# Kernel tuning notes

Measured on AMD Instinct MI355X. Metric: run time of the kernel, lower is better.

## Reference

```python
import jax, jax.numpy as jnp
import numpy as np

EMBED_DIM = 128
N_HEADS = 8
HEAD_DEPTH = EMBED_DIM // N_HEADS  # 16
CLIP = 10.0
B, N = 256, 1000


def setup_inputs() -> dict:
    key = jax.random.key(0)
    ks = jax.random.split(key, 10)
    D = EMBED_DIM
    return {
        "node_embeddings": jax.random.normal(ks[0], (B, N, D), jnp.float32),
        "graph_embedding": jax.random.normal(ks[1], (B, D), jnp.float32),
        "step_context": jax.random.normal(ks[2], (B, 1, D + 2), jnp.float32),
        "mask": jax.random.randint(ks[3], (B, 1, N), 0, 2).astype(bool),
        "Wk1": jax.random.normal(ks[4], (D, D), jnp.float32) / np.sqrt(D),
        "Wv": jax.random.normal(ks[5], (D, D), jnp.float32) / np.sqrt(D),
        "Wk2": jax.random.normal(ks[6], (D, D), jnp.float32) / np.sqrt(D),
        "Wq_fixed": jax.random.normal(ks[7], (D, D), jnp.float32) / np.sqrt(D),
        "Wout": jax.random.normal(ks[8], (D, D), jnp.float32) / np.sqrt(D),
        "Wq_step": jax.random.normal(ks[9], (D + 2, D), jnp.float32) / np.sqrt(D),
    }


def reference(node_embeddings, graph_embedding, step_context, mask,
              Wk1, Wv, Wk2, Wq_fixed, Wout, Wq_step):
    b, n, D = node_embeddings.shape
    H, dh = N_HEADS, HEAD_DEPTH
    neg_inf = jnp.float32(-1e9)

    # compute_static: precomputed projections of node/graph embeddings
    K1 = node_embeddings @ Wk1                      # [B,N,D]
    V = node_embeddings @ Wv                        # [B,N,D]
    K2 = node_embeddings @ Wk2                      # [B,N,D]
    Q_fixed = graph_embedding[:, None, :] @ Wq_fixed  # [B,1,D]

    # compute_dynamic: single-query masked MHA
    Q_step = step_context @ Wq_step                 # [B,1,D]
    Q1 = Q_fixed + Q_step                           # [B,1,D]
    q = Q1.reshape(b, 1, H, dh)
    k = K1.reshape(b, n, H, dh)
    v = V.reshape(b, n, H, dh)
    score = jnp.einsum('bqhd,bkhd->bhqk', q, k) / jnp.sqrt(jnp.float32(dh))
    score = jnp.where(mask[:, None, :, :], neg_inf, score)  # mask [B,1,N] -> [B,1,1,N]
    attn = jax.nn.softmax(score, axis=-1)           # [B,H,1,N]
    mha = jnp.einsum('bhqk,bkhd->bqhd', attn, v).reshape(b, 1, D)
    Q2 = mha @ Wout                                 # [B,1,D]

    # SHA: clipped single-head logits over all nodes
    logits = CLIP * jnp.tanh(
        jnp.einsum('bqd,bkd->bqk', Q2, K2) / jnp.sqrt(jnp.float32(D)))  # [B,1,N]
    logits = jnp.where(mask, neg_inf, logits)
    return logits[:, 0, :]                          # [B,N]
```

## Files before the change

### kernel.cpp

```cpp
#include <hip/hip_runtime.h>
#include <stdint.h>


#define DD 128
#define NH 8
#define DHD 16
#define NS 8
#define TILE 64
#define RP 132
#define SP 9
#define NMAX_PAD 1024

__device__ __forceinline__ bool detect_mask32(const void* maskp) {
    const uint32_t* mw = (const uint32_t*)maskp;
    bool m32 = true;
    #pragma unroll
    for (int i = 0; i < 16; ++i) m32 = m32 && (mw[i] <= 1u);
    return m32;
}

__global__ __launch_bounds__(128)
void k0_prep(const float* __restrict__ graph, const float* __restrict__ ctx,
             const float* __restrict__ Wk1, const float* __restrict__ Wqf,
             const float* __restrict__ Wqs, float* __restrict__ wq_ws)
{
    __shared__ float q1[DD];
    const int b = blockIdx.x, tid = threadIdx.x;
    const float* ge = graph + (size_t)b * DD;
    const float* sc = ctx + (size_t)b * (DD + 2);
    float acc = 0.f;
    #pragma unroll 4
    for (int k = 0; k < DD; ++k)     acc += ge[k] * Wqf[k * DD + tid];
    #pragma unroll 4
    for (int k = 0; k < DD + 2; ++k) acc += sc[k] * Wqs[k * DD + tid];
    q1[tid] = acc;
    __syncthreads();
    const float* wrow = Wk1 + (size_t)tid * DD;
    #pragma unroll
    for (int h = 0; h < NH; ++h) {
        float a = 0.f;
        #pragma unroll
        for (int j = 0; j < DHD; ++j) a += wrow[h * DHD + j] * q1[h * DHD + j];
        wq_ws[(size_t)b * NH * DD + h * DD + tid] = 0.25f * a;
    }
}

__global__ __launch_bounds__(512)
void kA_flash(const float* __restrict__ node, const float* __restrict__ wq_ws,
              const void* __restrict__ maskp, float* __restrict__ spart_ws,
              float* __restrict__ mz_ws, int N)
{
    __shared__ float tile[TILE * RP];
    __shared__ float wq_l[NH * RP];
    __shared__ float s_t[TILE * SP];
    const int b = blockIdx.y, j = blockIdx.x, tid = threadIdx.x;
    const int lane = tid & 63, h = tid >> 6;
    const int rows = (N + NS - 1) / NS;
    const int n0 = j * rows;
    const int nend = min(n0 + rows, N);
    const bool m32 = detect_mask32(maskp);
    const int32_t* mi = (const int32_t*)maskp + (size_t)b * N;
    const uint8_t* mb = (const uint8_t*)maskp + (size_t)b * N;
    const float* nodeB = node + (size_t)b * N * DD;

    for (int i = tid; i < NH * DD; i += 512)
        wq_l[(i >> 7) * RP + (i & 127)] = wq_ws[(size_t)b * NH * DD + i];

    const int r_sc = tid >> 3, h_sc = tid & 7;
    float m_run = -1e9f, z_run = 0.f;
    float accx = 0.f, accy = 0.f;

    const int ntiles = (nend - n0 + TILE - 1) / TILE;
    for (int t = 0; t < ntiles; ++t) {
        const int nt0 = n0 + t * TILE;
        #pragma unroll
        for (int c = 0; c < 4; ++c) {
            const int idx = c * 2048 + tid * 4;
            const int row = idx >> 7, col = idx & 127;
            if (nt0 + row < nend)
                *(float4*)&tile[row * RP + col] =
                    *(const float4*)(nodeB + (size_t)(nt0 + row) * DD + col);
        }
        __syncthreads();
        {
            const int n = nt0 + r_sc;
            float sc = -1e9f;
            if (n < nend) {
                const bool m = m32 ? (mi[n] != 0) : (mb[n] != 0);
                if (!m) {
                    const float4* nr = (const float4*)&tile[r_sc * RP];
                    const float4* wr = (const float4*)&wq_l[h_sc * RP];
                    float a = 0.f;
                    #pragma unroll
                    for (int k = 0; k < 32; ++k) {
                        const float4 x = nr[k], w = wr[k];
                        a += x.x * w.x + x.y * w.y + x.z * w.z + x.w * w.w;
                    }
                    sc = a;
                }
            }
            s_t[r_sc * SP + h_sc] = sc;
        }
        __syncthreads();
        {
            float scl = s_t[lane * SP + h];
            float tmax = scl;
            #pragma unroll
            for (int d = 1; d < 64; d <<= 1) tmax = fmaxf(tmax, __shfl_xor(tmax, d));
            const float m_new = fmaxf(m_run, tmax);
            const float rescale = __expf(m_run - m_new);
            const float e = __expf(scl - m_new);
            s_t[lane * SP + h] = e;
            float zt = e;
            #pragma unroll
            for (int d = 1; d < 64; d <<= 1) zt += __shfl_xor(zt, d);
            z_run = z_run * rescale + zt;
            accx *= rescale;
            accy *= rescale;
            m_run = m_new;
        }
        #pragma unroll 8
        for (int r = 0; r < TILE; ++r) {
            const float ef = s_t[r * SP + h];
            const float2 v = *(const float2*)&tile[r * RP + 2 * lane];
            accx += ef * v.x;
            accy += ef * v.y;
        }
        __syncthreads();
    }
    float* vout = spart_ws + (((size_t)b * NS + j) * NH + h) * DD;
    vout[2 * lane]     = accx;
    vout[2 * lane + 1] = accy;
    if (lane == 0) {
        float* mzp = mz_ws + (((size_t)b * NS + j) * NH + h) * 2;
        mzp[0] = m_run;
        mzp[1] = z_run;
    }
}

__global__ __launch_bounds__(128)
void kB_combine(const float* __restrict__ spart_ws, const float* __restrict__ mz_ws,
                const float* __restrict__ Wv, const float* __restrict__ Wout,
                const float* __restrict__ Wk2, float* __restrict__ w2_ws)
{
    __shared__ float m_l[NH * NS], z_l[NH * NS], wt[NH * NS];
    __shared__ float s_l[NH * DD];
    __shared__ float mha_l[DD];
    __shared__ float q2_l[DD];
    const int b = blockIdx.x, tid = threadIdx.x;

    if (tid < NH * NS) {
        const int h = tid >> 3, j = tid & 7;
        const float* mzp = mz_ws + (((size_t)b * NS + j) * NH + h) * 2;
        m_l[h * NS + j] = mzp[0];
        z_l[h * NS + j] = mzp[1];
    }
    __syncthreads();
    if (tid < NH) {
        const int h = tid;
        float M = -1e30f;
        #pragma unroll
        for (int j = 0; j < NS; ++j) M = fmaxf(M, m_l[h * NS + j]);
        float w[NS], Z = 0.f;
        #pragma unroll
        for (int j = 0; j < NS; ++j) {
            w[j] = __expf(m_l[h * NS + j] - M);
            Z += z_l[h * NS + j] * w[j];
        }
        const float rz = 1.f / Z;
        #pragma unroll
        for (int j = 0; j < NS; ++j) wt[h * NS + j] = w[j] * rz;
    }
    __syncthreads();
    const float* sp = spart_ws + (size_t)b * NS * NH * DD;
    for (int o = tid; o < NH * DD; o += 128) {
        const int h = o >> 7;
        float s = 0.f;
        #pragma unroll
        for (int j = 0; j < NS; ++j)
            s += sp[(size_t)j * NH * DD + o] * wt[h * NS + j];
        s_l[o] = s;
    }
    __syncthreads();
    {
        const int h = tid >> 4;
        float a = 0.f;
        for (int dp = 0; dp < DD; ++dp) a += s_l[h * DD + dp] * Wv[dp * DD + tid];
        mha_l[tid] = a;
    }
    __syncthreads();
    {
        float a = 0.f;
        for (int e = 0; e < DD; ++e) a += mha_l[e] * Wout[e * DD + tid];
        q2_l[tid] = a;
    }
    __syncthreads();
    {
        const float4* row = (const float4*)(Wk2 + (size_t)tid * DD);
        float a = 0.f;
        #pragma unroll
        for (int k = 0; k < 32; ++k) {
            const float4 w = row[k];
            a += w.x * q2_l[4*k] + w.y * q2_l[4*k+1] + w.z * q2_l[4*k+2] + w.w * q2_l[4*k+3];
        }
        w2_ws[(size_t)b * DD + tid] = a * 0.08838834764831845f;
    }
}

__global__ __launch_bounds__(256)
void k5_logits(const float* __restrict__ node, const float* __restrict__ w2_ws,
               const void* __restrict__ maskp, float* __restrict__ out, int N)
{
    const int b = blockIdx.y, j = blockIdx.x, tid = threadIdx.x;
    const int rows = (N + NS - 1) / NS;
    const int n0 = j * rows;
    const int nend = min(n0 + rows, N);
    const bool m32 = detect_mask32(maskp);
    const int32_t* mi = (const int32_t*)maskp + (size_t)b * N;
    const uint8_t* mb = (const uint8_t*)maskp + (size_t)b * N;
    const int sub = tid & 7, rr = tid >> 3;

    const float4* wv = (const float4*)(w2_ws + (size_t)b * DD + sub * 16);
    const float4 w0 = wv[0], w1 = wv[1], w2v = wv[2], w3 = wv[3];
    const float* nodeB = node + (size_t)b * N * DD;
    float* outB = out + (size_t)b * N;

    for (int n = n0 + rr; n < nend; n += 32) {
        const float4* nr = (const float4*)(nodeB + (size_t)n * DD + sub * 16);
        const float4 a0 = nr[0], a1 = nr[1], a2 = nr[2], a3 = nr[3];
        float p = a0.x*w0.x + a0.y*w0.y + a0.z*w0.z + a0.w*w0.w
                + a1.x*w1.x + a1.y*w1.y + a1.z*w1.z + a1.w*w1.w
                + a2.x*w2v.x + a2.y*w2v.y + a2.z*w2v.z + a2.w*w2v.w
                + a3.x*w3.x + a3.y*w3.y + a3.z*w3.z + a3.w*w3.w;
        p += __shfl_xor(p, 1);
        p += __shfl_xor(p, 2);
        p += __shfl_xor(p, 4);
        if (sub == 0) {
            const bool m = m32 ? (mi[n] != 0) : (mb[n] != 0);
            const float t = 1.f - 2.f / (__expf(2.f * p) + 1.f);
            outB[n] = m ? -1e9f : 10.f * t;
        }
    }
}

#define TPB 512
#define NMAX 1000
#define SPAD 9

__global__ __launch_bounds__(TPB)
void decoder_fallback(const float* __restrict__ node, const float* __restrict__ graph,
                      const float* __restrict__ ctx, const void* __restrict__ maskp,
                      const float* __restrict__ Wk1, const float* __restrict__ Wv,
                      const float* __restrict__ Wk2, const float* __restrict__ Wqf,
                      const float* __restrict__ Wout, const float* __restrict__ Wqs,
                      float* __restrict__ out, int N)
{
    __shared__ float node_tile[TILE * RP];
    __shared__ float scores[NMAX * SPAD];
    __shared__ float wq[NH * RP];
    __shared__ float s_lds[NH * RP];
    __shared__ float q1[DD];
    __shared__ float mha[DD];
    __shared__ float q2[DD];
    __shared__ float w2[DD];

    const int b = blockIdx.x, tid = threadIdx.x, lane = tid & 63, wave = tid >> 6;
    const bool mask32 = detect_mask32(maskp);
    const int32_t* mi = (const int32_t*)maskp + (size_t)b * N;
    const uint8_t* mb = (const uint8_t*)maskp + (size_t)b * N;
    const float* nodeB = node + (size_t)b * N * DD;

    if (tid < DD) {
        const float* ge = graph + (size_t)b * DD;
        const float* sc = ctx + (size_t)b * (DD + 2);
        float acc = 0.f;
        for (int k = 0; k < DD; ++k)     acc += ge[k] * Wqf[k * DD + tid];
        for (int k = 0; k < DD + 2; ++k) acc += sc[k] * Wqs[k * DD + tid];
        q1[tid] = acc;
    }
    __syncthreads();
    for (int idx = tid; idx < NH * DD; idx += TPB) {
        const int h = idx >> 7, dp = idx & (DD - 1);
        const float* wrow = Wk1 + dp * DD + h * DHD;
        float acc = 0.f;
        #pragma unroll
        for (int j = 0; j < DHD; ++j) acc += wrow[j] * q1[h * DHD + j];
        wq[h * RP + dp] = 0.25f * acc;
    }
    __syncthreads();
    const int ntiles = (N + TILE - 1) / TILE;
    const int n_local = tid >> 3, hA = tid & 7;
    for (int t = 0; t < ntiles; ++t) {
        const int n0 = t * TILE;
        #pragma unroll
        for (int c = 0; c < 4; ++c) {
            const int idx = c * (TPB * 4) + tid * 4;
            const int row = idx >> 7, col = idx & (DD - 1);
            if (n0 + row < N)
                *(float4*)&node_tile[row * RP + col] =
                    *(const float4*)(nodeB + (size_t)(n0 + row) * DD + col);
        }
        __syncthreads();
        if (n0 + n_local < N) {
            const float4* nr = (const float4*)&node_tile[n_local * RP];
            const float4* wr = (const float4*)&wq[hA * RP];
            float acc = 0.f;
            #pragma unroll
            for (int k = 0; k < DD / 4; ++k) {
                const float4 a = nr[k], w = wr[k];
                acc += a.x * w.x + a.y * w.y + a.z * w.z + a.w * w.w;
            }
            scores[(n0 + n_local) * SPAD + hA] = acc;
        }
        __syncthreads();
    }
    {
        const int h = wave;
        float sm[16];
        #pragma unroll
        for (int k = 0; k < 16; ++k) {
            const int n = lane + 64 * k;
            float v = -1e9f;
            if (n < N) {
                const bool m = mask32 ? (mi[n] != 0) : (mb[n] != 0);
                v = m ? -1e9f : scores[n * SPAD + h];
            }
            sm[k] = v;
        }
        float mx = sm[0];
        #pragma unroll
        for (int k = 1; k < 16; ++k) mx = fmaxf(mx, sm[k]);
        #pragma unroll
        for (int d = 1; d < 64; d <<= 1) mx = fmaxf(mx, __shfl_xor(mx, d));
        float e[16];
        float sum = 0.f;
        #pragma unroll
        for (int k = 0; k < 16; ++k) {
            const int n = lane + 64 * k;
            e[k] = (n < N) ? __expf(sm[k] - mx) : 0.f;
            sum += e[k];
        }
        #pragma unroll
        for (int d = 1; d < 64; d <<= 1) sum += __shfl_xor(sum, d);
        const float rinv = 1.f / sum;
        #pragma unroll
        for (int k = 0; k < 16; ++k) {
            const int n = lane + 64 * k;
            if (n < N) scores[n * SPAD + h] = e[k] * rinv;
        }
    }
    __syncthreads();
    {
        const int h = wave;
        const float2* n2 = (const float2*)nodeB;
        float a0 = 0.f, a1 = 0.f;
        #pragma unroll 4
        for (int n = 0; n < N; ++n) {
            const float at = scores[n * SPAD + h];
            const float2 v = n2[(size_t)n * 64 + lane];
            a0 += at * v.x;
            a1 += at * v.y;
        }
        s_lds[h * RP + 2 * lane] = a0;
        s_lds[h * RP + 2 * lane + 1] = a1;
    }
    __syncthreads();
    if (tid < DD) {
        const int h = tid >> 4;
        float acc = 0.f;
        for (int dp = 0; dp < DD; ++dp) acc += s_lds[h * RP + dp] * Wv[dp * DD + tid];
        mha[tid] = acc;
    }
    __syncthreads();
    if (tid < DD) {
        float acc = 0.f;
        for (int e = 0; e < DD; ++e) acc += mha[e] * Wout[e * DD + tid];
        q2[tid] = acc;
    }
    __syncthreads();
    if (tid < DD) {
        const float4* row = (const float4*)(Wk2 + tid * DD);
        float acc = 0.f;
        #pragma unroll
        for (int k = 0; k < DD / 4; ++k) {
            const float4 wv = row[k];
            acc += wv.x * q2[4*k] + wv.y * q2[4*k+1] + wv.z * q2[4*k+2] + wv.w * q2[4*k+3];
        }
        w2[tid] = acc * 0.08838834764831845f;
    }
    __syncthreads();
    {
        const float wa = w2[2 * lane], wb = w2[2 * lane + 1];
        const float2* n2 = (const float2*)nodeB;
        float* outB = out + (size_t)b * N;
        for (int n = wave; n < N; n += NH) {
            const float2 v = n2[(size_t)n * 64 + lane];
            float p = v.x * wa + v.y * wb;
            #pragma unroll
            for (int d = 1; d < 64; d <<= 1) p += __shfl_xor(p, d);
            if (lane == 0) {
                const bool m = mask32 ? (mi[n] != 0) : (mb[n] != 0);
                const float t = 1.f - 2.f / (__expf(2.f * p) + 1.f);
                outB[n] = m ? -1e9f : 10.f * t;
            }
        }
    }
}

extern "C" void kernel_launch(void* const* d_in, const int* in_sizes, int n_in,
                              void* d_out, int out_size, void* d_ws, size_t ws_size,
                              hipStream_t stream) {
    (void)n_in; (void)out_size;
    const float* node  = (const float*)d_in[0];
    const float* graph = (const float*)d_in[1];
    const float* ctx   = (const float*)d_in[2];
    const void*  mask  = d_in[3];
    const float* Wk1   = (const float*)d_in[4];
    const float* Wv    = (const float*)d_in[5];
    const float* Wk2   = (const float*)d_in[6];
    const float* Wqf   = (const float*)d_in[7];
    const float* Wout  = (const float*)d_in[8];
    const float* Wqs   = (const float*)d_in[9];

    const int B = in_sizes[1] / DD;
    const int N = in_sizes[0] / (B * DD);

    const size_t off_wq    = 0;
    const size_t off_spart = off_wq + (size_t)B * NH * DD;
    const size_t off_mz    = off_spart + (size_t)B * NS * NH * DD;
    const size_t off_w2    = off_mz + (size_t)B * NS * NH * 2;
    const size_t need_f    = off_w2 + (size_t)B * DD;

    if (N <= NMAX_PAD && ws_size >= need_f * sizeof(float)) {
        float* ws       = (float*)d_ws;
        float* wq_ws    = ws + off_wq;
        float* spart_ws = ws + off_spart;
        float* mz_ws    = ws + off_mz;
        float* w2_ws    = ws + off_w2;

        k0_prep<<<B, 128, 0, stream>>>(graph, ctx, Wk1, Wqf, Wqs, wq_ws);
        kA_flash<<<dim3(NS, B), 512, 0, stream>>>(node, wq_ws, mask, spart_ws, mz_ws, N);
        kB_combine<<<B, 128, 0, stream>>>(spart_ws, mz_ws, Wv, Wout, Wk2, w2_ws);
        k5_logits<<<dim3(NS, B), 256, 0, stream>>>(node, w2_ws, mask, (float*)d_out, N);
    } else {
        decoder_fallback<<<B, TPB, 0, stream>>>(node, graph, ctx, mask,
                                                Wk1, Wv, Wk2, Wqf, Wout, Wqs,
                                                (float*)d_out, N);
    }
}
```

Baseline: 118.6 us.

## Rewrite attention split kernel with bf16 MFMA for scores and PV

Replaces the scalar FP32 flash-style attention partial kernel with one that converts the node tile to bf16 in shared memory and uses 16x16x32 bf16 MFMA instructions for both the Q·K scores and the softmax-weighted V sum. Each block now loads its whole 125-row chunk at once and does a single-pass softmax with block-wide max and sum reductions, instead of an online rescaling loop over 64-row tiles. The goal is to move the FP32 ALU dot products onto matrix cores. In exchange, scores and probabilities are rounded to bf16, the code assumes at most 128 rows per split, and the transposed B-fragment gather for PV reads shared memory with strided scalar loads.

```diff
diff --git a/kernel.cpp b/kernel.cpp
--- a/kernel.cpp
+++ b/kernel.cpp
@@ -10,6 +10,15 @@
 #define RP 132
 #define SP 9
 #define NMAX_PAD 1024
+
+typedef short v8s __attribute__((ext_vector_type(8)));
+typedef float v4f __attribute__((ext_vector_type(4)));
+
+__device__ __forceinline__ unsigned short f2bf(float x) {
+    unsigned u = __float_as_uint(x);
+    u += 0x7fffu + ((u >> 16) & 1u);
+    return (unsigned short)(u >> 16);
+}
 
 __device__ __forceinline__ bool detect_mask32(const void* maskp) {
     const uint32_t* mw = (const uint32_t*)maskp;
@@ -46,95 +55,164 @@
 }
 
 __global__ __launch_bounds__(512)
-void kA_flash(const float* __restrict__ node, const float* __restrict__ wq_ws,
-              const void* __restrict__ maskp, float* __restrict__ spart_ws,
-              float* __restrict__ mz_ws, int N)
+void kA_mfma(const float* __restrict__ node, const float* __restrict__ wq_ws,
+             const void* __restrict__ maskp, float* __restrict__ spart_ws,
+             float* __restrict__ mz_ws, int N)
 {
-    __shared__ float tile[TILE * RP];
-    __shared__ float wq_l[NH * RP];
-    __shared__ float s_t[TILE * SP];
+    __shared__ __align__(16) unsigned short tA[2][8][64][16];
+    __shared__ __align__(16) unsigned short Ph[2][16][72];
+    __shared__ float wmax[16][9];
+    __shared__ float zpart[16][9];
+    __shared__ float mfin[16];
+
     const int b = blockIdx.y, j = blockIdx.x, tid = threadIdx.x;
-    const int lane = tid & 63, h = tid >> 6;
+    const int lane = tid & 63, w = tid >> 6;
+    const int c = lane & 15, g = lane >> 4;
     const int rows = (N + NS - 1) / NS;
     const int n0 = j * rows;
     const int nend = min(n0 + rows, N);
+
+    if (nend <= n0) {
+        float* sp = spart_ws + ((size_t)b * NS + j) * NH * DD;
+        for (int o = tid; o < NH * DD; o += 512) sp[o] = 0.f;
+        if (tid < NH) {
+            float* mzp = mz_ws + (((size_t)b * NS + j) * NH + tid) * 2;
+            mzp[0] = -1e30f; mzp[1] = 0.f;
+        }
+        return;
+    }
+
     const bool m32 = detect_mask32(maskp);
     const int32_t* mi = (const int32_t*)maskp + (size_t)b * N;
     const uint8_t* mb = (const uint8_t*)maskp + (size_t)b * N;
     const float* nodeB = node + (size_t)b * N * DD;
 
-    for (int i = tid; i < NH * DD; i += 512)
-        wq_l[(i >> 7) * RP + (i & 127)] = wq_ws[(size_t)b * NH * DD + i];
-
-    const int r_sc = tid >> 3, h_sc = tid & 7;
-    float m_run = -1e9f, z_run = 0.f;
-    float accx = 0.f, accy = 0.f;
-
-    const int ntiles = (nend - n0 + TILE - 1) / TILE;
-    for (int t = 0; t < ntiles; ++t) {
-        const int nt0 = n0 + t * TILE;
-        #pragma unroll
-        for (int c = 0; c < 4; ++c) {
-            const int idx = c * 2048 + tid * 4;
-            const int row = idx >> 7, col = idx & 127;
-            if (nt0 + row < nend)
-                *(float4*)&tile[row * RP + col] =
-                    *(const float4*)(nodeB + (size_t)(nt0 + row) * DD + col);
-        }
-        __syncthreads();
-        {
-            const int n = nt0 + r_sc;
-            float sc = -1e9f;
+    v8s aw[4];
+    #pragma unroll
+    for (int kk = 0; kk < 4; ++kk) {
+        v8s a;
+        #pragma unroll
+        for (int i = 0; i < 8; ++i) a[i] = 0;
+        if (c < NH) {
+            const float* wr = wq_ws + (size_t)b * NH * DD + (size_t)c * DD + kk * 32 + g * 8;
+            #pragma unroll
+            for (int i = 0; i < 8; ++i) a[i] = (short)f2bf(wr[i]);
+        }
+        aw[kk] = a;
+    }
+
+    {
+        const int L = tid >> 3, c8 = tid & 7;
+        #pragma unroll
+        for (int t = 0; t < 2; ++t) {
+            const int n = n0 + t * 64 + L;
+            unsigned short tmp[16];
             if (n < nend) {
-                const bool m = m32 ? (mi[n] != 0) : (mb[n] != 0);
-                if (!m) {
-                    const float4* nr = (const float4*)&tile[r_sc * RP];
-                    const float4* wr = (const float4*)&wq_l[h_sc * RP];
-                    float a = 0.f;
-                    #pragma unroll
-                    for (int k = 0; k < 32; ++k) {
-                        const float4 x = nr[k], w = wr[k];
-                        a += x.x * w.x + x.y * w.y + x.z * w.z + x.w * w.w;
-                    }
-                    sc = a;
+                const float4* src = (const float4*)(nodeB + (size_t)n * DD + c8 * 16);
+                #pragma unroll
+                for (int k = 0; k < 4; ++k) {
+                    const float4 v = src[k];
+                    tmp[4*k+0] = f2bf(v.x); tmp[4*k+1] = f2bf(v.y);
+                    tmp[4*k+2] = f2bf(v.z); tmp[4*k+3] = f2bf(v.w);
                 }
+            } else {
+                #pragma unroll
+                for (int k = 0; k < 16; ++k) tmp[k] = 0;
             }
-            s_t[r_sc * SP + h_sc] = sc;
-        }
-        __syncthreads();
-        {
-            float scl = s_t[lane * SP + h];
-            float tmax = scl;
-            #pragma unroll
-            for (int d = 1; d < 64; d <<= 1) tmax = fmaxf(tmax, __shfl_xor(tmax, d));
-            const float m_new = fmaxf(m_run, tmax);
-            const float rescale = __expf(m_run - m_new);
-            const float e = __expf(scl - m_new);
-            s_t[lane * SP + h] = e;
-            float zt = e;
-            #pragma unroll
-            for (int d = 1; d < 64; d <<= 1) zt += __shfl_xor(zt, d);
-            z_run = z_run * rescale + zt;
-            accx *= rescale;
-            accy *= rescale;
-            m_run = m_new;
-        }
-        #pragma unroll 8
-        for (int r = 0; r < TILE; ++r) {
-            const float ef = s_t[r * SP + h];
-            const float2 v = *(const float2*)&tile[r * RP + 2 * lane];
-            accx += ef * v.x;
-            accy += ef * v.y;
-        }
-        __syncthreads();
-    }
-    float* vout = spart_ws + (((size_t)b * NS + j) * NH + h) * DD;
-    vout[2 * lane]     = accx;
-    vout[2 * lane + 1] = accy;
-    if (lane == 0) {
-        float* mzp = mz_ws + (((size_t)b * NS + j) * NH + h) * 2;
-        mzp[0] = m_run;
-        mzp[1] = z_run;
+            *(v8s*)&tA[t][c8][L][0] = *(v8s*)&tmp[0];
+            *(v8s*)&tA[t][c8][L][8] = *(v8s*)&tmp[8];
+        }
+    }
+    __syncthreads();
+
+    const int ts = w >> 2, rg = w & 3;
+    const int nrow = n0 + ts * 64 + rg * 16 + c;
+    v4f sc = {0.f, 0.f, 0.f, 0.f};
+    #pragma unroll
+    for (int kk = 0; kk < 4; ++kk) {
+        const v8s bfrag = *(const v8s*)&tA[ts][kk * 2 + (g >> 1)][rg * 16 + c][(g & 1) * 8];
+        sc = __builtin_amdgcn_mfma_f32_16x16x32_bf16(aw[kk], bfrag, sc, 0, 0, 0);
+    }
+
+    float s4[4];
+    {
+        const bool valid = nrow < nend;
+        const bool msk = valid && (m32 ? (mi[nrow] != 0) : (mb[nrow] != 0));
+        #pragma unroll
+        for (int r = 0; r < 4; ++r)
+            s4[r] = !valid ? -1e30f : (msk ? -1e9f : sc[r]);
+    }
+
+    {
+        float mx[4];
+        #pragma unroll
+        for (int r = 0; r < 4; ++r) mx[r] = s4[r];
+        #pragma unroll
+        for (int d = 1; d < 16; d <<= 1) {
+            #pragma unroll
+            for (int r = 0; r < 4; ++r) mx[r] = fmaxf(mx[r], __shfl_xor(mx[r], d));
+        }
+        if (c == 0) {
+            #pragma unroll
+            for (int r = 0; r < 4; ++r) wmax[g * 4 + r][w] = mx[r];
+        }
+    }
+    __syncthreads();
+    if (w == 0 && lane < 16) {
+        float m = wmax[lane][0];
+        #pragma unroll
+        for (int ww = 1; ww < 8; ++ww) m = fmaxf(m, wmax[lane][ww]);
+        mfin[lane] = m;
+    }
+    __syncthreads();
+
+    {
+        float e4[4];
+        #pragma unroll
+        for (int r = 0; r < 4; ++r) e4[r] = __expf(s4[r] - mfin[g * 4 + r]);
+        float zr[4];
+        #pragma unroll
+        for (int r = 0; r < 4; ++r) zr[r] = e4[r];
+        #pragma unroll
+        for (int d = 1; d < 16; d <<= 1) {
+            #pragma unroll
+            for (int r = 0; r < 4; ++r) zr[r] += __shfl_xor(zr[r], d);
+        }
+        if (c == 0) {
+            #pragma unroll
+            for (int r = 0; r < 4; ++r) zpart[g * 4 + r][w] = zr[r];
+        }
+        #pragma unroll
+        for (int r = 0; r < 4; ++r)
+            Ph[ts][g * 4 + r][rg * 16 + c] = f2bf(e4[r]);
+    }
+    __syncthreads();
+
+    v4f c2 = {0.f, 0.f, 0.f, 0.f};
+    #pragma unroll
+    for (int s = 0; s < 4; ++s) {
+        const int t2 = s >> 1, s1 = s & 1;
+        const v8s pa = *(const v8s*)&Ph[t2][c][s1 * 32 + g * 8];
+        v8s bb;
+        #pragma unroll
+        for (int i = 0; i < 8; ++i)
+            bb[i] = (short)tA[t2][w][s1 * 32 + g * 8 + i][c];
+        c2 = __builtin_amdgcn_mfma_f32_16x16x32_bf16(pa, bb, c2, 0, 0, 0);
+    }
+
+    if (g < 2) {
+        float* sp = spart_ws + ((size_t)b * NS + j) * NH * DD;
+        #pragma unroll
+        for (int r = 0; r < 4; ++r)
+            sp[(g * 4 + r) * DD + w * 16 + c] = c2[r];
+    }
+    if (w == 0 && lane < NH) {
+        float z = 0.f;
+        #pragma unroll
+        for (int ww = 0; ww < 8; ++ww) z += zpart[lane][ww];
+        float* mzp = mz_ws + (((size_t)b * NS + j) * NH + lane) * 2;
+        mzp[0] = mfin[lane];
+        mzp[1] = z;
     }
 }
 
@@ -293,8 +371,8 @@
     for (int t = 0; t < ntiles; ++t) {
         const int n0 = t * TILE;
         #pragma unroll
-        for (int c = 0; c < 4; ++c) {
-            const int idx = c * (TPB * 4) + tid * 4;
+        for (int cc = 0; cc < 4; ++cc) {
+            const int idx = cc * (TPB * 4) + tid * 4;
             const int row = idx >> 7, col = idx & (DD - 1);
             if (n0 + row < N)
                 *(float4*)&node_tile[row * RP + col] =
@@ -307,8 +385,8 @@
             float acc = 0.f;
             #pragma unroll
             for (int k = 0; k < DD / 4; ++k) {
-                const float4 a = nr[k], w = wr[k];
-                acc += a.x * w.x + a.y * w.y + a.z * w.z + a.w * w.w;
+                const float4 a = nr[k], wv = wr[k];
+                acc += a.x * wv.x + a.y * wv.y + a.z * wv.z + a.w * wv.w;
             }
             scores[(n0 + n_local) * SPAD + hA] = acc;
         }
@@ -439,7 +517,7 @@
         float* w2_ws    = ws + off_w2;
 
         k0_prep<<<B, 128, 0, stream>>>(graph, ctx, Wk1, Wqf, Wqs, wq_ws);
-        kA_flash<<<dim3(NS, B), 512, 0, stream>>>(node, wq_ws, mask, spart_ws, mz_ws, N);
+        kA_mfma<<<dim3(NS, B), 512, 0, stream>>>(node, wq_ws, mask, spart_ws, mz_ws, N);
         kB_combine<<<B, 128, 0, stream>>>(spart_ws, mz_ws, Wv, Wout, Wk2, w2_ws);
         k5_logits<<<dim3(NS, B), 256, 0, stream>>>(node, w2_ws, mask, (float*)d_out, N);
     } else {
```

Result: faster. 97.45 us (-17.8%).
